# Performance work log

Hardware: AMD Instinct MI355X
Metric: run time of the kernel (lower is better)

## Reference

```python
import jax, jax.numpy as jnp
import numpy as np

N_NODES = 20000
N_EDGES = 200000
D_IN, D_H1, D_H2, D_OUT = 1433, 1000, 500, 7


def setup_inputs() -> dict:
    key = jax.random.key(0)
    ks = jax.random.split(key, 8)
    features = jax.random.normal(ks[0], (N_NODES, D_IN), dtype=jnp.float32)
    src = jax.random.randint(ks[1], (N_EDGES,), 0, N_NODES)
    dst = jax.random.randint(ks[2], (N_EDGES,), 0, N_NODES)
    W1 = jax.random.normal(ks[3], (D_IN, D_H1), dtype=jnp.float32) * 0.02
    b1 = jnp.zeros((D_H1,), dtype=jnp.float32)
    W2 = jax.random.normal(ks[4], (D_H1, D_H2), dtype=jnp.float32) * 0.02
    b2 = jnp.zeros((D_H2,), dtype=jnp.float32)
    W3 = jax.random.normal(ks[5], (D_H2, D_OUT), dtype=jnp.float32) * 0.02
    b3 = jnp.zeros((D_OUT,), dtype=jnp.float32)
    return {"features": features, "src": src, "dst": dst,
            "W1": W1, "b1": b1, "W2": W2, "b2": b2, "W3": W3, "b3": b3}


def reference(features, src, dst, W1, b1, W2, b2, W3, b3):
    N = features.shape[0]

    def agg(x):  # sum_tensors over incoming neighbors: h_i = sum_{(j->i) in E} x_j
        return jax.ops.segment_sum(x[src], dst, num_segments=N)

    # GCN layer 1: aggregate -> linear -> relu
    x = jax.nn.relu(agg(features) @ W1 + b1)       # [N, 1000]
    # GCN layer 2: aggregate -> linear -> relu (dropout = identity in eval)
    x = jax.nn.relu(agg(x) @ W2 + b2)              # [N, 500]
    # output linear -> relu (dropout = identity in eval)
    x = jax.nn.relu(x @ W3 + b3)                   # [N, 7]
    return x
```

## Files before the change

kernel.cpp:

```cpp
#include <hip/hip_runtime.h>
#include <hip/hip_bf16.h>


#define N_NODES 20000
#define N_EDGES 200000
#define D_IN    1433
#define D_H1    1000
#define D_H2    500
#define D_OUT   7

#define MPAD    20096
#define K1PAD   1472
#define N1PAD   1024
#define K2PAD   1024
#define N2PAD   512
#define H1STR   1008
#define H2STR   504
#define MBLK    157

typedef __attribute__((ext_vector_type(8))) short short8;
typedef __attribute__((ext_vector_type(8))) unsigned short ushort8_t;
typedef __attribute__((ext_vector_type(4))) float f32x4;

__device__ __forceinline__ unsigned short bf16_rne(float x) {
    unsigned int u = __float_as_uint(x);
    u = (u + 0x7FFFu + ((u >> 16) & 1u)) >> 16;
    return (unsigned short)u;
}
__device__ __forceinline__ float bf16_up(unsigned short h) {
    return __uint_as_float((unsigned int)h << 16);
}

__device__ __forceinline__ void gl_lds16(const unsigned short* g, unsigned short* lds) {
    __builtin_amdgcn_global_load_lds(
        (const __attribute__((address_space(1))) unsigned int*)g,
        (__attribute__((address_space(3))) unsigned int*)lds, 16, 0, 0);
}

__global__ __launch_bounds__(256) void count_deg(const int* __restrict__ dst,
                                                 int* __restrict__ offs) {
    int e = blockIdx.x * 256 + threadIdx.x;
    if (e < N_EDGES) atomicAdd(&offs[dst[e] + 1], 1);
}

__global__ __launch_bounds__(1024) void scan_csr(int* __restrict__ offs,
                                                 int* __restrict__ cursor, int n) {
    __shared__ int wsum[16];
    __shared__ int s_carry;
    const int t = threadIdx.x, lane = t & 63, wv = t >> 6;
    if (t == 0) s_carry = 0;
    __syncthreads();
    for (int base = 0; base < n; base += 1024) {
        int i = base + t;
        int v = (i < n) ? offs[i] : 0;
        #pragma unroll
        for (int s = 1; s < 64; s <<= 1) {
            int u = __shfl_up(v, s, 64);
            if (lane >= s) v += u;
        }
        if (lane == 63) wsum[wv] = v;
        __syncthreads();
        int prefix = s_carry;
        for (int k = 0; k < wv; ++k) prefix += wsum[k];
        v += prefix;
        if (i < n) {
            offs[i] = v;
            if (i < N_NODES) cursor[i] = v;
        }
        __syncthreads();
        if (t == 1023) s_carry = v;
    }
}

__global__ __launch_bounds__(256) void fill_csr(const int* __restrict__ src,
                                                const int* __restrict__ dst,
                                                int* __restrict__ cursor,
                                                int* __restrict__ srcs) {
    int e = blockIdx.x * 256 + threadIdx.x;
    if (e < N_EDGES) {
        int pos = atomicAdd(&cursor[dst[e]], 1);
        srcs[pos] = src[e];
    }
}

__global__ __launch_bounds__(256) void cast_features(const float* __restrict__ F,
                                                     unsigned int* __restrict__ out) {
    int row = blockIdx.x;
    int t = threadIdx.x;
    const float* fr = F + (size_t)row * D_IN;
    bool live = row < N_NODES;
    for (int kk = t; kk < K1PAD / 2; kk += 256) {
        int k0 = kk * 2;
        float a = (live && k0     < D_IN) ? fr[k0]     : 0.f;
        float b = (live && k0 + 1 < D_IN) ? fr[k0 + 1] : 0.f;
        out[(size_t)row * (K1PAD / 2) + kk] =
            (unsigned int)bf16_rne(a) | ((unsigned int)bf16_rne(b) << 16);
    }
}

template <int SR, int SC, int DR, int DC>
__global__ __launch_bounds__(256) void transpose_cast_pad(const float* __restrict__ src,
                                                          unsigned short* __restrict__ dst) {
    __shared__ float tile[32][33];
    int c0 = blockIdx.x * 32;
    int r0 = blockIdx.y * 32;
    int tx = threadIdx.x & 31, ty = threadIdx.x >> 5;
    #pragma unroll
    for (int p = 0; p < 4; ++p) {
        int r = r0 + ty + p * 8, c = c0 + tx;
        tile[ty + p * 8][tx] = (r < SR && c < SC) ? src[(size_t)r * SC + c] : 0.f;
    }
    __syncthreads();
    #pragma unroll
    for (int p = 0; p < 4; ++p) {
        int dr = c0 + ty + p * 8;
        int dc = r0 + tx;
        if (dr < DR && dc < DC) dst[(size_t)dr * DC + dc] = bf16_rne(tile[tx][ty + p * 8]);
    }
}

template <int KPAD, int NB>
__global__ __launch_bounds__(256) void gemm_mfma(const unsigned short* __restrict__ A,
                                                 const unsigned short* __restrict__ B,
                                                 unsigned short* __restrict__ C,
                                                 int M, int N, int OSTR) {
    __shared__ __align__(16) unsigned short sA[128 * 64];
    __shared__ __align__(16) unsigned short sB[128 * 64];
    const int bid = blockIdx.x;
    const int xcd = bid & 7;
    const int tt  = bid >> 3;
    const int nb  = tt % NB;
    const int mb  = (tt / NB) * 8 + xcd;
    if (mb >= MBLK) return;

    const int t = threadIdx.x;
    const int w = t >> 6, lane = t & 63;
    const int m0 = mb * 128, n0 = nb * 128;
    const int wm = (w >> 1) * 64, wn = (w & 1) * 64;

    const int srowo = lane >> 3;
    const int skc   = ((lane & 7) ^ srowo) * 8;
    const int mrow = lane & 15, quad = lane >> 4;

    const unsigned short* Aptr = A + (size_t)(m0 + srowo) * KPAD + skc;
    const unsigned short* Bptr = B + (size_t)(n0 + srowo) * KPAD + skc;

    f32x4 acc[4][4] = {};

    for (int k0 = 0; k0 < KPAD; k0 += 64) {
        #pragma unroll
        for (int c = 0; c < 4; ++c) {
            const int rbase = c * 32 + w * 8;
            gl_lds16(Aptr + (size_t)rbase * KPAD, &sA[rbase * 64]);
            gl_lds16(Bptr + (size_t)rbase * KPAD, &sB[rbase * 64]);
        }
        Aptr += 64; Bptr += 64;
        __syncthreads();

        #pragma unroll
        for (int s = 0; s < 2; ++s) {
            short8 af[4], bf[4];
            #pragma unroll
            for (int mt = 0; mt < 4; ++mt) {
                int r = wm + mt * 16 + mrow;
                af[mt] = *(const short8*)&sA[r * 64 + (((s * 4 + quad) ^ (mrow & 7)) * 8)];
            }
            #pragma unroll
            for (int nt = 0; nt < 4; ++nt) {
                int r = wn + nt * 16 + mrow;
                bf[nt] = *(const short8*)&sB[r * 64 + (((s * 4 + quad) ^ (mrow & 7)) * 8)];
            }
            #pragma unroll
            for (int mt = 0; mt < 4; ++mt)
                #pragma unroll
                for (int nt = 0; nt < 4; ++nt)
                    acc[mt][nt] = __builtin_amdgcn_mfma_f32_16x16x32_bf16(
                        af[mt], bf[nt], acc[mt][nt], 0, 0, 0);
        }
        __syncthreads();
    }

    #pragma unroll
    for (int mt = 0; mt < 4; ++mt) {
        int m = m0 + wm + mt * 16 + quad * 4;
        #pragma unroll
        for (int nt = 0; nt < 4; ++nt) {
            int n = n0 + wn + nt * 16 + mrow;
            if (n >= N) continue;
            #pragma unroll
            for (int r = 0; r < 4; ++r)
                if (m + r < M) C[(size_t)(m + r) * OSTR + n] = bf16_rne(acc[mt][nt][r]);
        }
    }
}

__global__ __launch_bounds__(128) void agg1_bf16(const unsigned short* __restrict__ H,
                                                 const int* __restrict__ offs,
                                                 const int* __restrict__ srcs,
                                                 const float* __restrict__ bias,
                                                 unsigned short* __restrict__ X) {
    const int i = blockIdx.x, t = threadIdx.x;
    const bool active = t < 125;
    const int tc = active ? t : 124;
    ushort8_t o = (ushort8_t)0;
    if (i < N_NODES) {
        const int beg = offs[i], end = offs[i + 1];
        const unsigned short* Hc = H + tc * 8;
        float s[8] = {};
        int e = beg;
        for (; e + 4 <= end; e += 4) {
            int j0 = srcs[e], j1 = srcs[e + 1], j2 = srcs[e + 2], j3 = srcs[e + 3];
            ushort8_t v0 = *(const ushort8_t*)(Hc + (size_t)j0 * H1STR);
            ushort8_t v1 = *(const ushort8_t*)(Hc + (size_t)j1 * H1STR);
            ushort8_t v2 = *(const ushort8_t*)(Hc + (size_t)j2 * H1STR);
            ushort8_t v3 = *(const ushort8_t*)(Hc + (size_t)j3 * H1STR);
            #pragma unroll
            for (int u = 0; u < 8; ++u)
                s[u] += (bf16_up(v0[u]) + bf16_up(v1[u])) +
                        (bf16_up(v2[u]) + bf16_up(v3[u]));
        }
        for (; e < end; ++e) {
            ushort8_t v = *(const ushort8_t*)(Hc + (size_t)srcs[e] * H1STR);
            #pragma unroll
            for (int u = 0; u < 8; ++u) s[u] += bf16_up(v[u]);
        }
        if (active) {
            #pragma unroll
            for (int u = 0; u < 8; ++u)
                o[u] = bf16_rne(fmaxf(s[u] + bias[t * 8 + u], 0.f));
        }
    }
    *(ushort8_t*)(X + (size_t)i * K2PAD + t * 8) = o;
}

__global__ __launch_bounds__(128) void agg2_out(const unsigned short* __restrict__ H,
                                                const int* __restrict__ offs,
                                                const int* __restrict__ srcs,
                                                const float* __restrict__ b2,
                                                const float* __restrict__ W3,
                                                const float* __restrict__ b3,
                                                float* __restrict__ out) {
    __shared__ float red[2][8];
    const int i = blockIdx.x, t = threadIdx.x;
    const bool active = t < 125;
    const int tc = active ? t : 124;
    const int beg = offs[i], end = offs[i + 1];
    const unsigned short* Hc = H + tc * 4;
    float s[4] = {};
    int e = beg;
    for (; e + 4 <= end; e += 4) {
        int j0 = srcs[e], j1 = srcs[e + 1], j2 = srcs[e + 2], j3 = srcs[e + 3];
        ushort4 v0 = *(const ushort4*)(Hc + (size_t)j0 * H2STR);
        ushort4 v1 = *(const ushort4*)(Hc + (size_t)j1 * H2STR);
        ushort4 v2 = *(const ushort4*)(Hc + (size_t)j2 * H2STR);
        ushort4 v3 = *(const ushort4*)(Hc + (size_t)j3 * H2STR);
        s[0] += (bf16_up(v0.x) + bf16_up(v1.x)) + (bf16_up(v2.x) + bf16_up(v3.x));
        s[1] += (bf16_up(v0.y) + bf16_up(v1.y)) + (bf16_up(v2.y) + bf16_up(v3.y));
        s[2] += (bf16_up(v0.z) + bf16_up(v1.z)) + (bf16_up(v2.z) + bf16_up(v3.z));
        s[3] += (bf16_up(v0.w) + bf16_up(v1.w)) + (bf16_up(v2.w) + bf16_up(v3.w));
    }
    for (; e < end; ++e) {
        ushort4 v = *(const ushort4*)(Hc + (size_t)srcs[e] * H2STR);
        s[0] += bf16_up(v.x); s[1] += bf16_up(v.y);
        s[2] += bf16_up(v.z); s[3] += bf16_up(v.w);
    }
    float acc[D_OUT] = {};
    if (active) {
        #pragma unroll
        for (int u = 0; u < 4; ++u) {
            float x = fmaxf(s[u] + b2[t * 4 + u], 0.f);
            const float* wr = W3 + (size_t)(t * 4 + u) * D_OUT;
            #pragma unroll
            for (int j = 0; j < D_OUT; ++j) acc[j] += x * wr[j];
        }
    }
    #pragma unroll
    for (int j = 0; j < D_OUT; ++j)
        #pragma unroll
        for (int off = 32; off; off >>= 1) acc[j] += __shfl_down(acc[j], off);
    const int lane = t & 63, wave = t >> 6;
    if (lane == 0) {
        #pragma unroll
        for (int j = 0; j < D_OUT; ++j) red[wave][j] = acc[j];
    }
    __syncthreads();
    if (t == 0) {
        #pragma unroll
        for (int j = 0; j < D_OUT; ++j)
            out[(size_t)i * D_OUT + j] = fmaxf(red[0][j] + red[1][j] + b3[j], 0.f);
    }
}

extern "C" void kernel_launch(void* const* d_in, const int* in_sizes, int n_in,
                              void* d_out, int out_size, void* d_ws, size_t ws_size,
                              hipStream_t stream) {
    const float* features = (const float*)d_in[0];
    const int*   src      = (const int*)d_in[1];
    const int*   dst      = (const int*)d_in[2];
    const float* W1       = (const float*)d_in[3];
    const float* b1       = (const float*)d_in[4];
    const float* W2       = (const float*)d_in[5];
    const float* b2       = (const float*)d_in[6];
    const float* W3       = (const float*)d_in[7];
    const float* b3       = (const float*)d_in[8];
    float* out = (float*)d_out;

    char* ws = (char*)d_ws;
    unsigned short* Fbf  = (unsigned short*)(ws + 0);
    unsigned short* X1bf = (unsigned short*)(ws + 0);
    unsigned short* H1   = (unsigned short*)(ws + 59162624);
    unsigned short* H2   = (unsigned short*)(ws + 59162624);
    unsigned short* W1T  = (unsigned short*)(ws + 99482624);
    unsigned short* W2T  = (unsigned short*)(ws + 102497280);
    int* offs   = (int*)(ws + 103545856);
    int* cursor = (int*)(ws + 103625984);
    int* srcs   = (int*)(ws + 103706112);

    hipMemsetAsync(offs, 0, (N_NODES + 1) * sizeof(int), stream);
    count_deg<<<(N_EDGES + 255) / 256, 256, 0, stream>>>(dst, offs);
    scan_csr<<<1, 1024, 0, stream>>>(offs, cursor, N_NODES + 1);
    fill_csr<<<(N_EDGES + 255) / 256, 256, 0, stream>>>(src, dst, cursor, srcs);

    cast_features<<<MPAD, 256, 0, stream>>>(features, (unsigned int*)Fbf);
    transpose_cast_pad<D_IN, D_H1, N1PAD, K1PAD>
        <<<dim3(N1PAD / 32, K1PAD / 32), 256, 0, stream>>>(W1, W1T);
    transpose_cast_pad<D_H1, D_H2, N2PAD, K2PAD>
        <<<dim3(N2PAD / 32, K2PAD / 32), 256, 0, stream>>>(W2, W2T);

    gemm_mfma<K1PAD, N1PAD / 128><<<8 * (N1PAD / 128) * 20, 256, 0, stream>>>(
        Fbf, W1T, H1, N_NODES, D_H1, H1STR);
    agg1_bf16<<<MPAD, 128, 0, stream>>>(H1, offs, srcs, b1, X1bf);

    gemm_mfma<K2PAD, N2PAD / 128><<<8 * (N2PAD / 128) * 20, 256, 0, stream>>>(
        X1bf, W2T, H2, N_NODES, D_H2, H2STR);
    agg2_out<<<N_NODES, 128, 0, stream>>>(H2, offs, srcs, b2, W3, b3, out);
}
```

Measured before the change: 436.2 us.

## Parallelize CSR scan, fuse degree count into cast, widen aggregation gathers

Replaces the single-block serial prefix scan with a three-kernel multi-block scan and fuses edge degree counting into the feature cast kernel. Both aggregation kernels unroll the neighbor gather by eight for more loads in flight. The second aggregation runs as one 64-thread wave with 8-wide loads, which removes the LDS reduction and barrier. The GEMM store now writes the padded columns up to the stride, which are zero because the weights are zero-padded.

```diff
diff --git a/kernel.cpp b/kernel.cpp
--- a/kernel.cpp
+++ b/kernel.cpp
@@ -17,6 +17,8 @@
 #define H1STR   1008
 #define H2STR   504
 #define MBLK    157
+#define SCAN_N  (N_NODES + 1)
+#define SCAN_NB 20
 
 typedef __attribute__((ext_vector_type(8))) short short8;
 typedef __attribute__((ext_vector_type(8))) unsigned short ushort8_t;
@@ -37,38 +39,66 @@
         (__attribute__((address_space(3))) unsigned int*)lds, 16, 0, 0);
 }
 
-__global__ __launch_bounds__(256) void count_deg(const int* __restrict__ dst,
-                                                 int* __restrict__ offs) {
-    int e = blockIdx.x * 256 + threadIdx.x;
+__global__ __launch_bounds__(256) void cast_count(const float* __restrict__ F,
+                                                  unsigned int* __restrict__ out,
+                                                  const int* __restrict__ dst,
+                                                  int* __restrict__ offs) {
+    int row = blockIdx.x;
+    int t = threadIdx.x;
+    int e = row * 256 + t;
     if (e < N_EDGES) atomicAdd(&offs[dst[e] + 1], 1);
-}
-
-__global__ __launch_bounds__(1024) void scan_csr(int* __restrict__ offs,
-                                                 int* __restrict__ cursor, int n) {
+    const float* fr = F + (size_t)row * D_IN;
+    bool live = row < N_NODES;
+    for (int kk = t; kk < K1PAD / 2; kk += 256) {
+        int k0 = kk * 2;
+        float a = (live && k0     < D_IN) ? fr[k0]     : 0.f;
+        float b = (live && k0 + 1 < D_IN) ? fr[k0 + 1] : 0.f;
+        out[(size_t)row * (K1PAD / 2) + kk] =
+            (unsigned int)bf16_rne(a) | ((unsigned int)bf16_rne(b) << 16);
+    }
+}
+
+__global__ __launch_bounds__(1024) void scan_part(int* __restrict__ offs,
+                                                  int* __restrict__ bsum) {
     __shared__ int wsum[16];
-    __shared__ int s_carry;
     const int t = threadIdx.x, lane = t & 63, wv = t >> 6;
-    if (t == 0) s_carry = 0;
+    int i = blockIdx.x * 1024 + t;
+    int v = (i < SCAN_N) ? offs[i] : 0;
+    #pragma unroll
+    for (int s = 1; s < 64; s <<= 1) {
+        int u = __shfl_up(v, s, 64);
+        if (lane >= s) v += u;
+    }
+    if (lane == 63) wsum[wv] = v;
     __syncthreads();
-    for (int base = 0; base < n; base += 1024) {
-        int i = base + t;
-        int v = (i < n) ? offs[i] : 0;
-        #pragma unroll
-        for (int s = 1; s < 64; s <<= 1) {
-            int u = __shfl_up(v, s, 64);
-            if (lane >= s) v += u;
-        }
-        if (lane == 63) wsum[wv] = v;
-        __syncthreads();
-        int prefix = s_carry;
-        for (int k = 0; k < wv; ++k) prefix += wsum[k];
-        v += prefix;
-        if (i < n) {
-            offs[i] = v;
-            if (i < N_NODES) cursor[i] = v;
-        }
-        __syncthreads();
-        if (t == 1023) s_carry = v;
+    int prefix = 0;
+    for (int k = 0; k < wv; ++k) prefix += wsum[k];
+    v += prefix;
+    if (i < SCAN_N) offs[i] = v;
+    if (t == 1023) bsum[blockIdx.x] = v;
+}
+
+__global__ __launch_bounds__(64) void scan_sums(int* __restrict__ bsum) {
+    const int t = threadIdx.x;
+    int v = (t < SCAN_NB) ? bsum[t] : 0;
+    #pragma unroll
+    for (int s = 1; s < 64; s <<= 1) {
+        int u = __shfl_up(v, s, 64);
+        if (t >= s) v += u;
+    }
+    if (t < SCAN_NB) bsum[t] = v;
+}
+
+__global__ __launch_bounds__(1024) void scan_add(int* __restrict__ offs,
+                                                 const int* __restrict__ bsum,
+                                                 int* __restrict__ cursor) {
+    int blk = blockIdx.x;
+    int i = blk * 1024 + threadIdx.x;
+    int add = blk ? bsum[blk - 1] : 0;
+    if (i < SCAN_N) {
+        int v = offs[i] + add;
+        offs[i] = v;
+        if (i < N_NODES) cursor[i] = v;
     }
 }
 
@@ -83,21 +113,6 @@
     }
 }
 
-__global__ __launch_bounds__(256) void cast_features(const float* __restrict__ F,
-                                                     unsigned int* __restrict__ out) {
-    int row = blockIdx.x;
-    int t = threadIdx.x;
-    const float* fr = F + (size_t)row * D_IN;
-    bool live = row < N_NODES;
-    for (int kk = t; kk < K1PAD / 2; kk += 256) {
-        int k0 = kk * 2;
-        float a = (live && k0     < D_IN) ? fr[k0]     : 0.f;
-        float b = (live && k0 + 1 < D_IN) ? fr[k0 + 1] : 0.f;
-        out[(size_t)row * (K1PAD / 2) + kk] =
-            (unsigned int)bf16_rne(a) | ((unsigned int)bf16_rne(b) << 16);
-    }
-}
-
 template <int SR, int SC, int DR, int DC>
 __global__ __launch_bounds__(256) void transpose_cast_pad(const float* __restrict__ src,
                                                           unsigned short* __restrict__ dst) {
@@ -123,7 +138,7 @@
 __global__ __launch_bounds__(256) void gemm_mfma(const unsigned short* __restrict__ A,
                                                  const unsigned short* __restrict__ B,
                                                  unsigned short* __restrict__ C,
-                                                 int M, int N, int OSTR) {
+                                                 int M, int OSTR) {
     __shared__ __align__(16) unsigned short sA[128 * 64];
     __shared__ __align__(16) unsigned short sB[128 * 64];
     const int bid = blockIdx.x;
@@ -186,7 +201,7 @@
         #pragma unroll
         for (int nt = 0; nt < 4; ++nt) {
             int n = n0 + wn + nt * 16 + mrow;
-            if (n >= N) continue;
+            if (n >= OSTR) continue;
             #pragma unroll
             for (int r = 0; r < 4; ++r)
                 if (m + r < M) C[(size_t)(m + r) * OSTR + n] = bf16_rne(acc[mt][nt][r]);
@@ -208,6 +223,26 @@
         const unsigned short* Hc = H + tc * 8;
         float s[8] = {};
         int e = beg;
+        for (; e + 8 <= end; e += 8) {
+            int j0 = srcs[e],     j1 = srcs[e + 1], j2 = srcs[e + 2], j3 = srcs[e + 3];
+            int j4 = srcs[e + 4], j5 = srcs[e + 5], j6 = srcs[e + 6], j7 = srcs[e + 7];
+            ushort8_t v0 = *(const ushort8_t*)(Hc + (size_t)j0 * H1STR);
+            ushort8_t v1 = *(const ushort8_t*)(Hc + (size_t)j1 * H1STR);
+            ushort8_t v2 = *(const ushort8_t*)(Hc + (size_t)j2 * H1STR);
+            ushort8_t v3 = *(const ushort8_t*)(Hc + (size_t)j3 * H1STR);
+            ushort8_t v4 = *(const ushort8_t*)(Hc + (size_t)j4 * H1STR);
+            ushort8_t v5 = *(const ushort8_t*)(Hc + (size_t)j5 * H1STR);
+            ushort8_t v6 = *(const ushort8_t*)(Hc + (size_t)j6 * H1STR);
+            ushort8_t v7 = *(const ushort8_t*)(Hc + (size_t)j7 * H1STR);
+            #pragma unroll
+            for (int u = 0; u < 8; ++u) {
+                float t0 = (bf16_up(v0[u]) + bf16_up(v1[u])) +
+                           (bf16_up(v2[u]) + bf16_up(v3[u]));
+                float t1 = (bf16_up(v4[u]) + bf16_up(v5[u])) +
+                           (bf16_up(v6[u]) + bf16_up(v7[u]));
+                s[u] += t0 + t1;
+            }
+        }
         for (; e + 4 <= end; e += 4) {
             int j0 = srcs[e], j1 = srcs[e + 1], j2 = srcs[e + 2], j3 = srcs[e + 3];
             ushort8_t v0 = *(const ushort8_t*)(Hc + (size_t)j0 * H1STR);
@@ -233,61 +268,77 @@
     *(ushort8_t*)(X + (size_t)i * K2PAD + t * 8) = o;
 }
 
-__global__ __launch_bounds__(128) void agg2_out(const unsigned short* __restrict__ H,
-                                                const int* __restrict__ offs,
-                                                const int* __restrict__ srcs,
-                                                const float* __restrict__ b2,
-                                                const float* __restrict__ W3,
-                                                const float* __restrict__ b3,
-                                                float* __restrict__ out) {
-    __shared__ float red[2][8];
+__global__ __launch_bounds__(64) void agg2_out(const unsigned short* __restrict__ H,
+                                               const int* __restrict__ offs,
+                                               const int* __restrict__ srcs,
+                                               const float* __restrict__ b2,
+                                               const float* __restrict__ W3,
+                                               const float* __restrict__ b3,
+                                               float* __restrict__ out) {
     const int i = blockIdx.x, t = threadIdx.x;
-    const bool active = t < 125;
-    const int tc = active ? t : 124;
+    const int tc = t < 63 ? t : 62;
     const int beg = offs[i], end = offs[i + 1];
-    const unsigned short* Hc = H + tc * 4;
-    float s[4] = {};
+    const unsigned short* Hc = H + tc * 8;
+    float s[8] = {};
     int e = beg;
+    for (; e + 8 <= end; e += 8) {
+        int j0 = srcs[e],     j1 = srcs[e + 1], j2 = srcs[e + 2], j3 = srcs[e + 3];
+        int j4 = srcs[e + 4], j5 = srcs[e + 5], j6 = srcs[e + 6], j7 = srcs[e + 7];
+        ushort8_t v0 = *(const ushort8_t*)(Hc + (size_t)j0 * H2STR);
+        ushort8_t v1 = *(const ushort8_t*)(Hc + (size_t)j1 * H2STR);
+        ushort8_t v2 = *(const ushort8_t*)(Hc + (size_t)j2 * H2STR);
+        ushort8_t v3 = *(const ushort8_t*)(Hc + (size_t)j3 * H2STR);
+        ushort8_t v4 = *(const ushort8_t*)(Hc + (size_t)j4 * H2STR);
+        ushort8_t v5 = *(const ushort8_t*)(Hc + (size_t)j5 * H2STR);
+        ushort8_t v6 = *(const ushort8_t*)(Hc + (size_t)j6 * H2STR);
+        ushort8_t v7 = *(const ushort8_t*)(Hc + (size_t)j7 * H2STR);
+        #pragma unroll
+        for (int u = 0; u < 8; ++u) {
+            float t0 = (bf16_up(v0[u]) + bf16_up(v1[u])) +
+                       (bf16_up(v2[u]) + bf16_up(v3[u]));
+            float t1 = (bf16_up(v4[u]) + bf16_up(v5[u])) +
+                       (bf16_up(v6[u]) + bf16_up(v7[u]));
+            s[u] += t0 + t1;
+        }
+    }
     for (; e + 4 <= end; e += 4) {
         int j0 = srcs[e], j1 = srcs[e + 1], j2 = srcs[e + 2], j3 = srcs[e + 3];
-        ushort4 v0 = *(const ushort4*)(Hc + (size_t)j0 * H2STR);
-        ushort4 v1 = *(const ushort4*)(Hc + (size_t)j1 * H2STR);
-        ushort4 v2 = *(const ushort4*)(Hc + (size_t)j2 * H2STR);
-        ushort4 v3 = *(const ushort4*)(Hc + (size_t)j3 * H2STR);
-        s[0] += (bf16_up(v0.x) + bf16_up(v1.x)) + (bf16_up(v2.x) + bf16_up(v3.x));
-        s[1] += (bf16_up(v0.y) + bf16_up(v1.y)) + (bf16_up(v2.y) + bf16_up(v3.y));
-        s[2] += (bf16_up(v0.z) + bf16_up(v1.z)) + (bf16_up(v2.z) + bf16_up(v3.z));
-        s[3] += (bf16_up(v0.w) + bf16_up(v1.w)) + (bf16_up(v2.w) + bf16_up(v3.w));
+        ushort8_t v0 = *(const ushort8_t*)(Hc + (size_t)j0 * H2STR);
+        ushort8_t v1 = *(const ushort8_t*)(Hc + (size_t)j1 * H2STR);
+        ushort8_t v2 = *(const ushort8_t*)(Hc + (size_t)j2 * H2STR);
+        ushort8_t v3 = *(const ushort8_t*)(Hc + (size_t)j3 * H2STR);
+        #pragma unroll
+        for (int u = 0; u < 8; ++u)
+            s[u] += (bf16_up(v0[u]) + bf16_up(v1[u])) +
+                    (bf16_up(v2[u]) + bf16_up(v3[u]));
     }
     for (; e < end; ++e) {
-        ushort4 v = *(const ushort4*)(Hc + (size_t)srcs[e] * H2STR);
-        s[0] += bf16_up(v.x); s[1] += bf16_up(v.y);
-        s[2] += bf16_up(v.z); s[3] += bf16_up(v.w);
-    }
+        ushort8_t v = *(const ushort8_t*)(Hc + (size_t)srcs[e] * H2STR);
+        #pragma unroll
+        for (int u = 0; u < 8; ++u) s[u] += bf16_up(v[u]);
+    }
+
     float acc[D_OUT] = {};
-    if (active) {
-        #pragma unroll
-        for (int u = 0; u < 4; ++u) {
-            float x = fmaxf(s[u] + b2[t * 4 + u], 0.f);
-            const float* wr = W3 + (size_t)(t * 4 + u) * D_OUT;
-            #pragma unroll
-            for (int j = 0; j < D_OUT; ++j) acc[j] += x * wr[j];
+    if (t < 63) {
+        #pragma unroll
+        for (int u = 0; u < 8; ++u) {
+            int col = t * 8 + u;
+            if (col < D_H2) {
+                float x = fmaxf(s[u] + b2[col], 0.f);
+                const float* wr = W3 + (size_t)col * D_OUT;
+                #pragma unroll
+                for (int j = 0; j < D_OUT; ++j) acc[j] += x * wr[j];
+            }
         }
     }
     #pragma unroll
     for (int j = 0; j < D_OUT; ++j)
         #pragma unroll
         for (int off = 32; off; off >>= 1) acc[j] += __shfl_down(acc[j], off);
-    const int lane = t & 63, wave = t >> 6;
-    if (lane == 0) {
-        #pragma unroll
-        for (int j = 0; j < D_OUT; ++j) red[wave][j] = acc[j];
-    }
-    __syncthreads();
     if (t == 0) {
         #pragma unroll
         for (int j = 0; j < D_OUT; ++j)
-            out[(size_t)i * D_OUT + j] = fmaxf(red[0][j] + red[1][j] + b3[j], 0.f);
+            out[(size_t)i * D_OUT + j] = fmaxf(acc[j] + b3[j], 0.f);
     }
 }
 
@@ -315,23 +366,26 @@
     int* offs   = (int*)(ws + 103545856);
     int* cursor = (int*)(ws + 103625984);
     int* srcs   = (int*)(ws + 103706112);
+    int* bsum   = cursor + N_NODES;
 
     hipMemsetAsync(offs, 0, (N_NODES + 1) * sizeof(int), stream);
-    count_deg<<<(N_EDGES + 255) / 256, 256, 0, stream>>>(dst, offs);
-    scan_csr<<<1, 1024, 0, stream>>>(offs, cursor, N_NODES + 1);
-    fill_csr<<<(N_EDGES + 255) / 256, 256, 0, stream>>>(src, dst, cursor, srcs);
-
-    cast_features<<<MPAD, 256, 0, stream>>>(features, (unsigned int*)Fbf);
+
+    cast_count<<<MPAD, 256, 0, stream>>>(features, (unsigned int*)Fbf, dst, offs);
     transpose_cast_pad<D_IN, D_H1, N1PAD, K1PAD>
         <<<dim3(N1PAD / 32, K1PAD / 32), 256, 0, stream>>>(W1, W1T);
     transpose_cast_pad<D_H1, D_H2, N2PAD, K2PAD>
         <<<dim3(N2PAD / 32, K2PAD / 32), 256, 0, stream>>>(W2, W2T);
 
+    scan_part<<<SCAN_NB, 1024, 0, stream>>>(offs, bsum);
+    scan_sums<<<1, 64, 0, stream>>>(bsum);
+    scan_add<<<SCAN_NB, 1024, 0, stream>>>(offs, bsum, cursor);
+    fill_csr<<<(N_EDGES + 255) / 256, 256, 0, stream>>>(src, dst, cursor, srcs);
+
     gemm_mfma<K1PAD, N1PAD / 128><<<8 * (N1PAD / 128) * 20, 256, 0, stream>>>(
-        Fbf, W1T, H1, N_NODES, D_H1, H1STR);
+        Fbf, W1T, H1, N_NODES, H1STR);
     agg1_bf16<<<MPAD, 128, 0, stream>>>(H1, offs, srcs, b1, X1bf);
 
     gemm_mfma<K2PAD, N2PAD / 128><<<8 * (N2PAD / 128) * 20, 256, 0, stream>>>(
-        X1bf, W2T, H2, N_NODES, D_H2, H2STR);
-    agg2_out<<<N_NODES, 128, 0, stream>>>(H2, offs, srcs, b2, W3, b3, out);
-}
+        X1bf, W2T, H2, N_NODES, H2STR);
+    agg2_out<<<N_NODES, 64, 0, stream>>>(H2, offs, srcs, b2, W3, b3, out);
+}
```

Result: faster. 420.1 us (-3.7%).
